# Optimization experiments

Measured on AMD Instinct MI355X. Metric: run time of the kernel, lower is better.

The kernel has to match this reference:

```python
import jax, jax.numpy as jnp
import numpy as np
from jax import lax

B, T, N, D = 8, 256, 128, 16
H, Hb, K, L, OUT = 128, 64, 3, 8, 24  # L = num_stacks*layers_per_stack
DILS = [2 ** (i % 4) for i in range(L)]


def setup_inputs() -> dict:
    key = jax.random.key(0)
    ks = jax.random.split(key, 16)
    s = 0.05
    return {
        "x": jax.random.normal(ks[0], (B, T, N, D), jnp.float32),
        "in_w": jax.random.normal(ks[1], (D, H), jnp.float32) * s,
        "in_b": jnp.zeros((H,), jnp.float32),
        "pw_in_w": jax.random.normal(ks[2], (L, Hb, H), jnp.float32) * s,   # conv1x1 H->Hb
        "dw_w": jax.random.normal(ks[3], (L, 2 * Hb, 1, K), jnp.float32) * s,  # grouped conv, groups=Hb
        "pw_out_w": jax.random.normal(ks[4], (L, H, Hb), jnp.float32) * s,  # conv1x1 Hb->H
        "gn_g": jnp.ones((L, H), jnp.float32),
        "gn_b": jnp.zeros((L, H), jnp.float32),
        "skip_w": jax.random.normal(ks[5], (L, H, H), jnp.float32) * s,
        "ln_g": jnp.ones((H,), jnp.float32),
        "ln_b": jnp.zeros((H,), jnp.float32),
        "h1_w": jax.random.normal(ks[6], (H, H), jnp.float32) * s,
        "h1_b": jnp.zeros((H,), jnp.float32),
        "h2_w": jax.random.normal(ks[7], (H, OUT), jnp.float32) * s,
        "h2_b": jnp.zeros((OUT,), jnp.float32),
    }


def _group_norm1(x, g, b, eps=1e-5):
    # GroupNorm(num_groups=1, C): normalize over (C, T) per sample, per-channel affine
    m = jnp.mean(x, axis=(1, 2), keepdims=True)
    v = jnp.var(x, axis=(1, 2), keepdims=True)
    return (x - m) * lax.rsqrt(v + eps) * g[None, :, None] + b[None, :, None]


def reference(x, in_w, in_b, pw_in_w, dw_w, pw_out_w, gn_g, gn_b, skip_w,
              ln_g, ln_b, h1_w, h1_b, h2_w, h2_b):
    b, t, n, _ = x.shape
    h = x @ in_w + in_b                              # (B,T,N,H)
    z = h.transpose(0, 2, 3, 1).reshape(b * n, H, t)  # (B*N,H,T)
    skip_sum = jnp.zeros_like(z)
    for i, d in enumerate(DILS):
        u = jnp.einsum('bct,oc->bot', z, pw_in_w[i])  # pointwise H->Hb
        pad = (K - 1) * d
        u = jnp.pad(u, ((0, 0), (0, 0), (pad, 0)))   # causal left-pad
        v = lax.conv_general_dilated(
            u, dw_w[i], (1,), 'VALID', rhs_dilation=(d,),
            dimension_numbers=('NCH', 'OIH', 'NCH'), feature_group_count=Hb)
        f, gate = jnp.split(v, 2, axis=1)            # torch.chunk(z, 2, dim=1)
        w = jnp.tanh(f) * jax.nn.sigmoid(gate)       # GLU gate, (B*N,Hb,T)
        s_feat = jnp.einsum('bct,oc->bot', w, pw_out_w[i])  # Hb->H (dropout=identity in eval)
        z = _group_norm1(z + s_feat, gn_g[i], gn_b[i])
        skip_sum = skip_sum + jnp.einsum('bct,oc->bot', s_feat, skip_w[i])
    h_last = skip_sum[:, :, -1]                      # (B*N,H)
    mu = jnp.mean(h_last, -1, keepdims=True)
    var = jnp.var(h_last, -1, keepdims=True)
    hn = (h_last - mu) * lax.rsqrt(var + 1e-5) * ln_g + ln_b
    y = jax.nn.gelu(hn @ h1_w + h1_b, approximate=False) @ h2_w + h2_b  # (B*N,OUT)
    return y.reshape(b, n, OUT).transpose(0, 2, 1)   # (B,T_out,N)
```

## Files before the change

kernel.cpp:

```cpp
#include <hip/hip_runtime.h>
#include <hip/hip_fp16.h>
#include <math.h>

#define TT 256
#define HC 128
#define HB 64
#define NL 8

#define WS_PB  65536
#define WS_PG  66048
#define WS_GP  66560
#define WS_BP  67584

typedef _Float16 f16x8 __attribute__((ext_vector_type(8)));
typedef float f32x4 __attribute__((ext_vector_type(4)));

__device__ __forceinline__ f16x8 asf16x8(uint4 v) {
    union { uint4 u; f16x8 h; } cv; cv.u = v; return cv.h;
}
__device__ __forceinline__ f32x4 mfma16(uint4 a, uint4 b, f32x4 c) {
    return __builtin_amdgcn_mfma_f32_16x16x32_f16(asf16x8(a), asf16x8(b), c, 0, 0, 0);
}
__device__ __forceinline__ float fast_tanh(float x) {
    float e = __expf(2.f * fabsf(x));
    float r = 1.f - 2.f / (1.f + e);
    return copysignf(r, x);
}
__device__ __forceinline__ float fast_sig(float x) {
    return 1.f / (1.f + __expf(-x));
}
__device__ __forceinline__ unsigned packh2(float a, float b) {
    __half2 h = __floats2half2_rn(a, b);
    return __builtin_bit_cast(unsigned, h);
}
__device__ __forceinline__ float loh(unsigned u) {
    return __low2float(__builtin_bit_cast(__half2, u));
}
__device__ __forceinline__ float hih(unsigned u) {
    return __high2float(__builtin_bit_cast(__half2, u));
}
__device__ __forceinline__ unsigned u4get(uint4 v, int q) {
    return q == 0 ? v.x : q == 1 ? v.y : q == 2 ? v.z : v.w;
}

__global__ __launch_bounds__(256)
void tcn_setup(const float* __restrict__ pw_in, const float* __restrict__ pw_out,
               const float* __restrict__ gn_g, const float* __restrict__ gn_b,
               float* __restrict__ ws) {
    const int i = blockIdx.x;
    const int tid = threadIdx.x;
    uint4* WPA = (uint4*)ws;
    float* Pb = ws + WS_PB;
    float* Pg = ws + WS_PG;
    float* Gp = ws + WS_GP;
    float* Bp = ws + WS_BP;

    if (tid < HC) {
        float g  = (i == 0) ? 1.f : gn_g[(i - 1) * HC + tid];
        float bb = (i == 0) ? 0.f : gn_b[(i - 1) * HC + tid];
        Gp[i * HC + tid] = g;
        Bp[i * HC + tid] = bb;
    }
    for (int e = tid; e < 16 * 64; e += 256) {
        int tile = e >> 6, lane = e & 63;
        int mt = tile >> 2, kt = tile & 3;
        int o = 16 * mt + (lane & 15);
        int chb = 32 * kt + 8 * (lane >> 4);
        uint4 v;
        unsigned vq[4];
        for (int q = 0; q < 4; q++) {
            int ch = chb + 2 * q;
            float g0 = (i == 0) ? 1.f : gn_g[(i - 1) * HC + ch];
            float g1 = (i == 0) ? 1.f : gn_g[(i - 1) * HC + ch + 1];
            float w0 = pw_in[((size_t)i * HB + o) * HC + ch] * g0;
            float w1 = pw_in[((size_t)i * HB + o) * HC + ch + 1] * g1;
            vq[q] = packh2(w0, w1);
        }
        v.x = vq[0]; v.y = vq[1]; v.z = vq[2]; v.w = vq[3];
        WPA[((size_t)i * 16 + tile) * 64 + lane] = v;
    }
    for (int e = tid; e < 16 * 64; e += 256) {
        int tile = e >> 6, lane = e & 63;
        int ms = tile >> 1, ks = tile & 1;
        int o = 16 * ms + (lane & 15);
        int chb = 32 * ks + 8 * (lane >> 4);
        uint4 v;
        unsigned vq[4];
        for (int q = 0; q < 4; q++) {
            int ch = chb + 2 * q;
            float w0 = pw_out[((size_t)i * HC + o) * HB + ch];
            float w1 = pw_out[((size_t)i * HC + o) * HB + ch + 1];
            vq[q] = packh2(w0, w1);
        }
        v.x = vq[0]; v.y = vq[1]; v.z = vq[2]; v.w = vq[3];
        WPA[8192 + ((size_t)i * 16 + tile) * 64 + lane] = v;
    }
    if (tid < HB) {
        float pb = 0.f, pg = 0.f;
        for (int c = 0; c < HC; c++) {
            float w = pw_in[((size_t)i * HB + tid) * HC + c];
            float gc = (i == 0) ? 1.f : gn_g[(i - 1) * HC + c];
            float bc = (i == 0) ? 0.f : gn_b[(i - 1) * HC + c];
            pb += bc * w;
            pg += gc * w;
        }
        Pb[i * HB + tid] = pb;
        Pg[i * HB + tid] = pg;
    }
}

__global__ __launch_bounds__(256)
void tcn_main(const float* __restrict__ x, const float* __restrict__ in_w,
              const float* __restrict__ in_b, const float* __restrict__ dw_w,
              const float* __restrict__ pw_out, const float* __restrict__ skip_w,
              const float* __restrict__ ln_g, const float* __restrict__ ln_b,
              const float* __restrict__ h1_w, const float* __restrict__ h1_b,
              const float* __restrict__ h2_w, const float* __restrict__ h2_b,
              const float* __restrict__ ws, float* __restrict__ out) {
    __shared__ unsigned scratch[16 * 257];
    __shared__ unsigned haloB[3 * 32 * 17];
    __shared__ float sLast[NL * HC];
    __shared__ float red[16];
    float* hbuf = (float*)scratch;
    float* qbuf = hbuf + 128;

    const float* Pb = ws + WS_PB;
    const float* Pg = ws + WS_PG;
    const float* Gp = ws + WS_GP;
    const float* Bp = ws + WS_BP;
    const uint4* WPA = (const uint4*)ws;

    const int t = threadIdx.x;
    const int bn = blockIdx.x;
    const int b = bn >> 7, n = bn & 127;
    const int lane = t & 63;
    const int wv = t >> 6;
    const int cc = lane & 15;
    const int l4 = lane >> 4;

    unsigned z2[64];
    {
        const float* xp = x + (((size_t)b * TT + t) * 128 + n) * 16;
        float xr[16];
#pragma unroll
        for (int d = 0; d < 16; d++) xr[d] = xp[d];
#pragma unroll
        for (int c = 0; c < HC; c += 2) {
            float a0 = in_b[c], a1 = in_b[c + 1];
#pragma unroll
            for (int d = 0; d < 16; d++) {
                a0 = fmaf(xr[d], in_w[d * HC + c], a0);
                a1 = fmaf(xr[d], in_w[d * HC + c + 1], a1);
            }
            z2[c >> 1] = packh2(a0, a1);
        }
    }

    uint4 zB[4][4];
#pragma unroll
    for (int kt = 0; kt < 4; kt++) {
#pragma unroll
        for (int q = 0; q < 16; q++) scratch[q * 257 + t] = z2[16 * kt + q];
        __syncthreads();
#pragma unroll
        for (int nt = 0; nt < 4; nt++) {
            int col = 64 * wv + nt * 16 + cc;
            uint4 v;
            v.x = scratch[(4 * l4 + 0) * 257 + col];
            v.y = scratch[(4 * l4 + 1) * 257 + col];
            v.z = scratch[(4 * l4 + 2) * 257 + col];
            v.w = scratch[(4 * l4 + 3) * 257 + col];
            zB[kt][nt] = v;
        }
        __syncthreads();
    }

    float m_s = 0.f, r_s = 1.f;

#pragma unroll 1
    for (int L = 0; L < NL; L++) {
        const int dil = 1 << (L & 3), d1 = dil, d2 = 2 * dil;
        const bool lastL = (L == NL - 1);
        const bool act = (!lastL) || (wv == 3);
        const float mr = m_s * r_s;

        f32x4 cu[4][4];
        if (act) {
            const uint4* AU = WPA + (size_t)L * 16 * 64;
#pragma unroll
            for (int mt = 0; mt < 4; mt++) {
                uint4 a0 = AU[(mt * 4 + 0) * 64 + lane];
                uint4 a1 = AU[(mt * 4 + 1) * 64 + lane];
                uint4 a2 = AU[(mt * 4 + 2) * 64 + lane];
                uint4 a3 = AU[(mt * 4 + 3) * 64 + lane];
                float4 pbv = *(const float4*)(Pb + L * HB + 16 * mt + 4 * l4);
                float4 pgv = *(const float4*)(Pg + L * HB + 16 * mt + 4 * l4);
#pragma unroll
                for (int nt = 0; nt < 4; nt++) {
                    f32x4 acc = {0.f, 0.f, 0.f, 0.f};
                    acc = mfma16(a0, zB[0][nt], acc);
                    acc = mfma16(a1, zB[1][nt], acc);
                    acc = mfma16(a2, zB[2][nt], acc);
                    acc = mfma16(a3, zB[3][nt], acc);
                    acc[0] = fmaf(r_s, acc[0], pbv.x - mr * pgv.x);
                    acc[1] = fmaf(r_s, acc[1], pbv.y - mr * pgv.y);
                    acc[2] = fmaf(r_s, acc[2], pbv.z - mr * pgv.z);
                    acc[3] = fmaf(r_s, acc[3], pbv.w - mr * pgv.w);
                    cu[mt][nt] = acc;
                }
            }
            if (wv < 3) {
#pragma unroll
                for (int mt = 0; mt < 4; mt++)
#pragma unroll
                    for (int rp = 0; rp < 2; rp++)
                        haloB[wv * (32 * 17) + (8 * mt + 2 * l4 + rp) * 17 + cc] =
                            packh2(cu[mt][3][2 * rp], cu[mt][3][2 * rp + 1]);
            }
        }
        __syncthreads();

        unsigned bwv[2][4][4];
        if (act) {
            const float* dwl = dw_w + (size_t)L * 384;
#pragma unroll
            for (int mtf = 0; mtf < 2; mtf++) {
#pragma unroll
                for (int r = 0; r < 4; r++) {
                    const int o = 16 * mtf + 4 * l4 + r;
                    const float* df0 = dwl + (2 * o) * 3;
                    const float* df1 = dwl + (2 * o + 1) * 3;
                    const float* dg0 = dwl + (64 + 2 * o) * 3;
                    const float* dg1 = dwl + (64 + 2 * o + 1) * 3;
                    const int hrowf = (8 * mtf + 2 * l4 + (r >> 1)) * 17;
                    const int hrowg = (8 * (mtf + 2) + 2 * l4 + (r >> 1)) * 17;
                    const int hbase = (wv > 0 ? wv - 1 : 0) * (32 * 17);
#pragma unroll
                    for (int nt = 0; nt < 4; nt++) {
                        float uf = cu[mtf][nt][r];
                        float ug = cu[mtf + 2][nt][r];
                        float m1f, m1g, m2f, m2g;
                        {
                            const int cd = (cc - d1) & 15;
                            const int src = (lane & 48) | cd;
                            float sf = __shfl(uf, src), sg = __shfl(ug, src);
                            float pf, pg_;
                            if (nt > 0) {
                                pf  = __shfl(cu[mtf][nt - 1][r], src);
                                pg_ = __shfl(cu[mtf + 2][nt - 1][r], src);
                            } else {
                                unsigned hf = haloB[hbase + hrowf + cd];
                                unsigned hg = haloB[hbase + hrowg + cd];
                                pf  = (r & 1) ? hih(hf) : loh(hf);
                                pg_ = (r & 1) ? hih(hg) : loh(hg);
                                if (wv == 0) { pf = 0.f; pg_ = 0.f; }
                            }
                            bool in = (cc >= d1);
                            m1f = in ? sf : pf;  m1g = in ? sg : pg_;
                        }
                        {
                            const int cd = (cc - d2) & 15;
                            const int src = (lane & 48) | cd;
                            float sf = __shfl(uf, src), sg = __shfl(ug, src);
                            float pf, pg_;
                            if (nt > 0) {
                                pf  = __shfl(cu[mtf][nt - 1][r], src);
                                pg_ = __shfl(cu[mtf + 2][nt - 1][r], src);
                            } else {
                                unsigned hf = haloB[hbase + hrowf + cd];
                                unsigned hg = haloB[hbase + hrowg + cd];
                                pf  = (r & 1) ? hih(hf) : loh(hf);
                                pg_ = (r & 1) ? hih(hg) : loh(hg);
                                if (wv == 0) { pf = 0.f; pg_ = 0.f; }
                            }
                            bool in = (cc >= d2);
                            m2f = in ? sf : pf;  m2g = in ? sg : pg_;
                        }
                        float f0 = m2f * df0[0] + m1f * df0[1] + uf * df0[2];
                        float f1 = m2f * df1[0] + m1f * df1[1] + uf * df1[2];
                        float g0 = m2g * dg0[0] + m1g * dg0[1] + ug * dg0[2];
                        float g1 = m2g * dg1[0] + m1g * dg1[1] + ug * dg1[2];
                        bwv[mtf][nt][r] =
                            packh2(fast_tanh(f0) * fast_sig(g0), fast_tanh(f1) * fast_sig(g1));
                    }
                }
            }
        }

        float s1 = 0.f, s2 = 0.f;
        if (act) {
            uint4 Bw[2][4];
#pragma unroll
            for (int ks = 0; ks < 2; ks++)
#pragma unroll
                for (int nt = 0; nt < 4; nt++) {
                    uint4 v;
                    v.x = bwv[ks][nt][0]; v.y = bwv[ks][nt][1];
                    v.z = bwv[ks][nt][2]; v.w = bwv[ks][nt][3];
                    Bw[ks][nt] = v;
                }
            const uint4* AS = WPA + 8192 + (size_t)L * 16 * 64;
#pragma unroll
            for (int kt = 0; kt < 4; kt++) {
                f32x4 cs[2][4];
#pragma unroll
                for (int lo = 0; lo < 2; lo++) {
                    const int ms = 2 * kt + lo;
                    uint4 a0 = AS[(ms * 2 + 0) * 64 + lane];
                    uint4 a1 = AS[(ms * 2 + 1) * 64 + lane];
#pragma unroll
                    for (int nt = 0; nt < 4; nt++) {
                        f32x4 acc = {0.f, 0.f, 0.f, 0.f};
                        acc = mfma16(a0, Bw[0][nt], acc);
                        acc = mfma16(a1, Bw[1][nt], acc);
                        cs[lo][nt] = acc;
                    }
                }
                if (wv == 3 && cc == 15) {
#pragma unroll
                    for (int lo = 0; lo < 2; lo++)
#pragma unroll
                        for (int r = 0; r < 4; r++)
                            sLast[L * HC + 16 * (2 * kt + lo) + 4 * l4 + r] = cs[lo][3][r];
                }
                if (!lastL) {
                    const int losel = l4 >> 1;
#pragma unroll
                    for (int nt = 0; nt < 4; nt++) {
                        unsigned zp[4];
#pragma unroll
                        for (int q = 0; q < 4; q++) {
                            const int src = (((2 * l4 + (q >> 1)) & 3) << 4) | cc;
                            float v00 = __shfl(cs[0][nt][(2 * q) & 3], src);
                            float v01 = __shfl(cs[1][nt][(2 * q) & 3], src);
                            float sf0 = losel ? v01 : v00;
                            float v10 = __shfl(cs[0][nt][(2 * q + 1) & 3], src);
                            float v11 = __shfl(cs[1][nt][(2 * q + 1) & 3], src);
                            float sf1 = losel ? v11 : v10;
                            unsigned zold = u4get(zB[kt][nt], q);
                            float zo0 = loh(zold), zo1 = hih(zold);
                            float2 gv = *(const float2*)(Gp + L * HC + 32 * kt + 8 * l4 + 2 * q);
                            float2 bv = *(const float2*)(Bp + L * HC + 32 * kt + 8 * l4 + 2 * q);
                            float zn0 = fmaf(zo0, r_s * gv.x, (bv.x - mr * gv.x) + sf0);
                            float zn1 = fmaf(zo1, r_s * gv.y, (bv.y - mr * gv.y) + sf1);
                            zp[q] = packh2(zn0, zn1);
                            s1 += zn0 + zn1;
                            s2 += zn0 * zn0 + zn1 * zn1;
                        }
                        uint4 v;
                        v.x = zp[0]; v.y = zp[1]; v.z = zp[2]; v.w = zp[3];
                        zB[kt][nt] = v;
                    }
                }
            }
        }
        if (!lastL) {
#pragma unroll
            for (int off = 32; off; off >>= 1) {
                s1 += __shfl_xor(s1, off);
                s2 += __shfl_xor(s2, off);
            }
            if (lane == 0) { red[wv * 2] = s1; red[wv * 2 + 1] = s2; }
            __syncthreads();
            float S1 = red[0] + red[2] + red[4] + red[6];
            float S2 = red[1] + red[3] + red[5] + red[7];
            float mu = S1 * (1.f / 32768.f);
            float var = S2 * (1.f / 32768.f) - mu * mu;
            m_s = mu;
            r_s = rsqrtf(var + 1e-5f);
        }
    }
    __syncthreads();

    float hl = 0.f;
    if (t < HC) {
        for (int i = 0; i < NL; i++) {
            const float4* swr = (const float4*)(skip_w + (((size_t)i * HC) + t) * HC);
            const float* sl = sLast + i * HC;
#pragma unroll 4
            for (int c4 = 0; c4 < 32; c4++) {
                float4 sw = swr[c4];
                hl += sw.x * sl[4 * c4] + sw.y * sl[4 * c4 + 1] + sw.z * sl[4 * c4 + 2] + sw.w * sl[4 * c4 + 3];
            }
        }
        hbuf[t] = hl;
    }
    __syncthreads();
    if (t < 64) {
        float v0 = hbuf[t], v1 = hbuf[t + 64];
        float a = v0 + v1, q = v0 * v0 + v1 * v1;
#pragma unroll
        for (int off = 32; off; off >>= 1) {
            a += __shfl_xor(a, off);
            q += __shfl_xor(q, off);
        }
        if (t == 0) {
            float mu = a * (1.f / 128.f);
            red[0] = mu;
            red[1] = rsqrtf(q * (1.f / 128.f) - mu * mu + 1e-5f);
        }
    }
    __syncthreads();
    {
        float mu = red[0], rs = red[1];
        if (t < HC) hbuf[t] = (hl - mu) * rs * ln_g[t] + ln_b[t];
    }
    __syncthreads();
    if (t < HC) {
        float q = h1_b[t];
        for (int c = 0; c < HC; c++) q = fmaf(hbuf[c], h1_w[c * HC + t], q);
        q = 0.5f * q * (1.f + erff(q * 0.70710678118654752f));
        qbuf[t] = q;
    }
    __syncthreads();
    if (t < 24) {
        float o = h2_b[t];
        for (int c = 0; c < HC; c++) o = fmaf(qbuf[c], h2_w[c * 24 + t], o);
        out[((size_t)b * 24 + t) * 128 + n] = o;
    }
}

extern "C" void kernel_launch(void* const* d_in, const int* in_sizes, int n_in,
                              void* d_out, int out_size, void* d_ws, size_t ws_size,
                              hipStream_t stream) {
    const float* x      = (const float*)d_in[0];
    const float* in_w   = (const float*)d_in[1];
    const float* in_b   = (const float*)d_in[2];
    const float* pw_in  = (const float*)d_in[3];
    const float* dw_w   = (const float*)d_in[4];
    const float* pw_out = (const float*)d_in[5];
    const float* gn_g   = (const float*)d_in[6];
    const float* gn_b   = (const float*)d_in[7];
    const float* skip_w = (const float*)d_in[8];
    const float* ln_g   = (const float*)d_in[9];
    const float* ln_b   = (const float*)d_in[10];
    const float* h1_w   = (const float*)d_in[11];
    const float* h1_b   = (const float*)d_in[12];
    const float* h2_w   = (const float*)d_in[13];
    const float* h2_b   = (const float*)d_in[14];
    float* out = (float*)d_out;
    float* ws  = (float*)d_ws;

    tcn_setup<<<NL, 256, 0, stream>>>(pw_in, pw_out, gn_g, gn_b, ws);

    tcn_main<<<1024, 256, 0, stream>>>(x, in_w, in_b, dw_w, pw_out, skip_w,
                                       ln_g, ln_b, h1_w, h1_b, h2_w, h2_b, ws, out);
}
```

Measured before the change: 540.7 us.

## Pack conv inputs to fp16 pairs for shuffles and route skip-transpose through LDS

The pointwise-conv output is packed into half2 words right after the MFMA, so the dilated causal conv moves two channels per lane shuffle and uses a single select for the halo. This roughly halves the cross-lane shuffle count. The output-projection transpose, which used many shuffles per element, now goes through a per-wave LDS staging buffer, and scratch is enlarged to hold it. In exchange, s_feat and u are rounded to fp16 before the residual and conv, and extra LDS traffic is added.

```diff
diff --git a/kernel.cpp b/kernel.cpp
--- a/kernel.cpp
+++ b/kernel.cpp
@@ -117,7 +117,7 @@
               const float* __restrict__ h1_w, const float* __restrict__ h1_b,
               const float* __restrict__ h2_w, const float* __restrict__ h2_b,
               const float* __restrict__ ws, float* __restrict__ out) {
-    __shared__ unsigned scratch[16 * 257];
+    __shared__ unsigned scratch[4224];
     __shared__ unsigned haloB[3 * 32 * 17];
     __shared__ float sLast[NL * HC];
     __shared__ float red[16];
@@ -184,7 +184,7 @@
         const bool act = (!lastL) || (wv == 3);
         const float mr = m_s * r_s;
 
-        f32x4 cu[4][4];
+        unsigned pu[4][4][2];
         if (act) {
             const uint4* AU = WPA + (size_t)L * 16 * 64;
 #pragma unroll
@@ -202,11 +202,12 @@
                     acc = mfma16(a1, zB[1][nt], acc);
                     acc = mfma16(a2, zB[2][nt], acc);
                     acc = mfma16(a3, zB[3][nt], acc);
-                    acc[0] = fmaf(r_s, acc[0], pbv.x - mr * pgv.x);
-                    acc[1] = fmaf(r_s, acc[1], pbv.y - mr * pgv.y);
-                    acc[2] = fmaf(r_s, acc[2], pbv.z - mr * pgv.z);
-                    acc[3] = fmaf(r_s, acc[3], pbv.w - mr * pgv.w);
-                    cu[mt][nt] = acc;
+                    float u0 = fmaf(r_s, acc[0], pbv.x - mr * pgv.x);
+                    float u1 = fmaf(r_s, acc[1], pbv.y - mr * pgv.y);
+                    float u2 = fmaf(r_s, acc[2], pbv.z - mr * pgv.z);
+                    float u3 = fmaf(r_s, acc[3], pbv.w - mr * pgv.w);
+                    pu[mt][nt][0] = packh2(u0, u1);
+                    pu[mt][nt][1] = packh2(u2, u3);
                 }
             }
             if (wv < 3) {
@@ -214,8 +215,7 @@
                 for (int mt = 0; mt < 4; mt++)
 #pragma unroll
                     for (int rp = 0; rp < 2; rp++)
-                        haloB[wv * (32 * 17) + (8 * mt + 2 * l4 + rp) * 17 + cc] =
-                            packh2(cu[mt][3][2 * rp], cu[mt][3][2 * rp + 1]);
+                        haloB[wv * (32 * 17) + (8 * mt + 2 * l4 + rp) * 17 + cc] = pu[mt][3][rp];
             }
         }
         __syncthreads();
@@ -223,65 +223,66 @@
         unsigned bwv[2][4][4];
         if (act) {
             const float* dwl = dw_w + (size_t)L * 384;
+            const int hb = (wv > 0 ? wv - 1 : 0) * (32 * 17);
 #pragma unroll
             for (int mtf = 0; mtf < 2; mtf++) {
 #pragma unroll
-                for (int r = 0; r < 4; r++) {
-                    const int o = 16 * mtf + 4 * l4 + r;
-                    const float* df0 = dwl + (2 * o) * 3;
-                    const float* df1 = dwl + (2 * o + 1) * 3;
-                    const float* dg0 = dwl + (64 + 2 * o) * 3;
-                    const float* dg1 = dwl + (64 + 2 * o + 1) * 3;
-                    const int hrowf = (8 * mtf + 2 * l4 + (r >> 1)) * 17;
-                    const int hrowg = (8 * (mtf + 2) + 2 * l4 + (r >> 1)) * 17;
-                    const int hbase = (wv > 0 ? wv - 1 : 0) * (32 * 17);
+                for (int rp = 0; rp < 2; rp++) {
+                    unsigned hf = 0u, hg = 0u;
+                    if (wv > 0) {
+                        hf = haloB[hb + (8 * mtf + 2 * l4 + rp) * 17 + cc];
+                        hg = haloB[hb + (8 * (mtf + 2) + 2 * l4 + rp) * 17 + cc];
+                    }
+                    unsigned m1f[4], m1g[4], m2f[4], m2g[4];
+                    {
+                        const int srcl = (lane & 48) | ((cc - d1) & 15);
+                        const bool own = (cc <= 15 - d1);
+#pragma unroll
+                        for (int nt = 0; nt < 4; nt++) {
+                            unsigned wf = own ? pu[mtf][nt][rp]
+                                              : (nt > 0 ? pu[mtf][nt - 1][rp] : hf);
+                            unsigned wg = own ? pu[mtf + 2][nt][rp]
+                                              : (nt > 0 ? pu[mtf + 2][nt - 1][rp] : hg);
+                            m1f[nt] = __shfl(wf, srcl);
+                            m1g[nt] = __shfl(wg, srcl);
+                        }
+                    }
+                    {
+                        const int srcl = (lane & 48) | ((cc - d2) & 15);
+                        const bool own = (cc <= 15 - d2);
+#pragma unroll
+                        for (int nt = 0; nt < 4; nt++) {
+                            unsigned wf = own ? pu[mtf][nt][rp]
+                                              : (nt > 0 ? pu[mtf][nt - 1][rp] : hf);
+                            unsigned wg = own ? pu[mtf + 2][nt][rp]
+                                              : (nt > 0 ? pu[mtf + 2][nt - 1][rp] : hg);
+                            m2f[nt] = __shfl(wf, srcl);
+                            m2g[nt] = __shfl(wg, srcl);
+                        }
+                    }
+                    const int o = 16 * mtf + 4 * l4 + 2 * rp;
+                    const float* df = dwl + (2 * o) * 3;
+                    const float* dg = dwl + (64 + 2 * o) * 3;
 #pragma unroll
                     for (int nt = 0; nt < 4; nt++) {
-                        float uf = cu[mtf][nt][r];
-                        float ug = cu[mtf + 2][nt][r];
-                        float m1f, m1g, m2f, m2g;
-                        {
-                            const int cd = (cc - d1) & 15;
-                            const int src = (lane & 48) | cd;
-                            float sf = __shfl(uf, src), sg = __shfl(ug, src);
-                            float pf, pg_;
-                            if (nt > 0) {
-                                pf  = __shfl(cu[mtf][nt - 1][r], src);
-                                pg_ = __shfl(cu[mtf + 2][nt - 1][r], src);
-                            } else {
-                                unsigned hf = haloB[hbase + hrowf + cd];
-                                unsigned hg = haloB[hbase + hrowg + cd];
-                                pf  = (r & 1) ? hih(hf) : loh(hf);
-                                pg_ = (r & 1) ? hih(hg) : loh(hg);
-                                if (wv == 0) { pf = 0.f; pg_ = 0.f; }
-                            }
-                            bool in = (cc >= d1);
-                            m1f = in ? sf : pf;  m1g = in ? sg : pg_;
-                        }
-                        {
-                            const int cd = (cc - d2) & 15;
-                            const int src = (lane & 48) | cd;
-                            float sf = __shfl(uf, src), sg = __shfl(ug, src);
-                            float pf, pg_;
-                            if (nt > 0) {
-                                pf  = __shfl(cu[mtf][nt - 1][r], src);
-                                pg_ = __shfl(cu[mtf + 2][nt - 1][r], src);
-                            } else {
-                                unsigned hf = haloB[hbase + hrowf + cd];
-                                unsigned hg = haloB[hbase + hrowg + cd];
-                                pf  = (r & 1) ? hih(hf) : loh(hf);
-                                pg_ = (r & 1) ? hih(hg) : loh(hg);
-                                if (wv == 0) { pf = 0.f; pg_ = 0.f; }
-                            }
-                            bool in = (cc >= d2);
-                            m2f = in ? sf : pf;  m2g = in ? sg : pg_;
-                        }
-                        float f0 = m2f * df0[0] + m1f * df0[1] + uf * df0[2];
-                        float f1 = m2f * df1[0] + m1f * df1[1] + uf * df1[2];
-                        float g0 = m2g * dg0[0] + m1g * dg0[1] + ug * dg0[2];
-                        float g1 = m2g * dg1[0] + m1g * dg1[1] + ug * dg1[2];
-                        bwv[mtf][nt][r] =
+                        float uf0 = loh(pu[mtf][nt][rp]),     uf1 = hih(pu[mtf][nt][rp]);
+                        float ug0 = loh(pu[mtf + 2][nt][rp]), ug1 = hih(pu[mtf + 2][nt][rp]);
+                        float a1f0 = loh(m1f[nt]), a1f1 = hih(m1f[nt]);
+                        float a2f0 = loh(m2f[nt]), a2f1 = hih(m2f[nt]);
+                        float a1g0 = loh(m1g[nt]), a1g1 = hih(m1g[nt]);
+                        float a2g0 = loh(m2g[nt]), a2g1 = hih(m2g[nt]);
+                        float f0 = a2f0 * df[0] + a1f0 * df[1]  + uf0 * df[2];
+                        float f1 = a2f0 * df[3] + a1f0 * df[4]  + uf0 * df[5];
+                        float f2 = a2f1 * df[6] + a1f1 * df[7]  + uf1 * df[8];
+                        float f3 = a2f1 * df[9] + a1f1 * df[10] + uf1 * df[11];
+                        float g0 = a2g0 * dg[0] + a1g0 * dg[1]  + ug0 * dg[2];
+                        float g1 = a2g0 * dg[3] + a1g0 * dg[4]  + ug0 * dg[5];
+                        float g2 = a2g1 * dg[6] + a1g1 * dg[7]  + ug1 * dg[8];
+                        float g3 = a2g1 * dg[9] + a1g1 * dg[10] + ug1 * dg[11];
+                        bwv[mtf][nt][2 * rp] =
                             packh2(fast_tanh(f0) * fast_sig(g0), fast_tanh(f1) * fast_sig(g1));
+                        bwv[mtf][nt][2 * rp + 1] =
+                            packh2(fast_tanh(f2) * fast_sig(g2), fast_tanh(f3) * fast_sig(g3));
                     }
                 }
             }
@@ -300,6 +301,7 @@
                     Bw[ks][nt] = v;
                 }
             const uint4* AS = WPA + 8192 + (size_t)L * 16 * 64;
+            unsigned* SB = scratch + wv * (16 * 66);
 #pragma unroll
             for (int kt = 0; kt < 4; kt++) {
                 f32x4 cs[2][4];
@@ -324,19 +326,22 @@
                             sLast[L * HC + 16 * (2 * kt + lo) + 4 * l4 + r] = cs[lo][3][r];
                 }
                 if (!lastL) {
-                    const int losel = l4 >> 1;
+#pragma unroll
+                    for (int lo = 0; lo < 2; lo++)
+#pragma unroll
+                        for (int nt = 0; nt < 4; nt++) {
+                            SB[(8 * lo + 2 * l4 + 0) * 66 + 16 * nt + cc] =
+                                packh2(cs[lo][nt][0], cs[lo][nt][1]);
+                            SB[(8 * lo + 2 * l4 + 1) * 66 + 16 * nt + cc] =
+                                packh2(cs[lo][nt][2], cs[lo][nt][3]);
+                        }
 #pragma unroll
                     for (int nt = 0; nt < 4; nt++) {
                         unsigned zp[4];
 #pragma unroll
                         for (int q = 0; q < 4; q++) {
-                            const int src = (((2 * l4 + (q >> 1)) & 3) << 4) | cc;
-                            float v00 = __shfl(cs[0][nt][(2 * q) & 3], src);
-                            float v01 = __shfl(cs[1][nt][(2 * q) & 3], src);
-                            float sf0 = losel ? v01 : v00;
-                            float v10 = __shfl(cs[0][nt][(2 * q + 1) & 3], src);
-                            float v11 = __shfl(cs[1][nt][(2 * q + 1) & 3], src);
-                            float sf1 = losel ? v11 : v10;
+                            unsigned sp = SB[(4 * l4 + q) * 66 + 16 * nt + cc];
+                            float sf0 = loh(sp), sf1 = hih(sp);
                             unsigned zold = u4get(zB[kt][nt], q);
                             float zo0 = loh(zold), zo1 = hih(zold);
                             float2 gv = *(const float2*)(Gp + L * HC + 32 * kt + 8 * l4 + 2 * q);
```

Result: faster. 488.9 us (-9.6%).
